# Kernel tuning notes

Hardware: AMD Instinct MI355X
Metric: run time of the kernel (lower is better)

## Reference

```python
import math
import jax, jax.numpy as jnp
import numpy as np

D = 2048
NH = 16
HD = D // NH
B_IMG = 32
H_ORIG, W_ORIG = 28, 36
POOL = 2
HF, WF = H_ORIG // POOL, W_ORIG // POOL  # 14, 18
T = HF * WF                              # 252 tokens per image
S_TOTAL = B_IMG * T                      # 8064
EPS = 1e-6


def setup_inputs() -> dict:
    key = jax.random.key(0)
    ks = jax.random.split(key, 12)
    w = lambda k, shp: jax.random.normal(k, shp, dtype=jnp.float32) * 0.02
    return {
        'semantic_hidden': jax.random.normal(ks[0], (1, S_TOTAL, D), jnp.float32),
        'vggt_features': jax.random.normal(ks[1], (1, S_TOTAL, D), jnp.float32),
        'grid_thw': jnp.tile(jnp.array([[1, H_ORIG, W_ORIG]], dtype=jnp.int64), (B_IMG, 1)),
        'ln1_w': jnp.ones((D,), jnp.float32), 'ln1_b': jnp.zeros((D,), jnp.float32),
        'ln2_w': jnp.ones((D,), jnp.float32), 'ln2_b': jnp.zeros((D,), jnp.float32),
        'Wq': w(ks[2], (D, D)), 'Wk': w(ks[3], (D, D)),
        'Wv': w(ks[4], (D, D)), 'Wo': w(ks[5], (D, D)),
        'imp_w1': w(ks[6], (D // 4, D)), 'imp_b1': jnp.zeros((D // 4,), jnp.float32),
        'imp_w2': w(ks[7], (1, D // 4)), 'imp_b2': jnp.zeros((1,), jnp.float32),
        'gate_w': w(ks[8], (NH // 2, D)), 'gate_b': jnp.zeros((NH // 2,), jnp.float32),
        'gate': jnp.asarray(0.5, jnp.float32),  # torch init is 0.0 (output would be all-zero); use 0.5 for a meaningful baseline
    }


def _layernorm(x, w, b):
    mu = jnp.mean(x, axis=-1, keepdims=True)
    var = jnp.var(x, axis=-1, keepdims=True)
    return (x - mu) * jax.lax.rsqrt(var + EPS) * w + b


def _spatial_bias(h_feat, w_feat, dtype):
    y = jnp.arange(h_feat, dtype=dtype)
    x = jnp.arange(w_feat, dtype=dtype)
    gy, gx = jnp.meshgrid(y, x, indexing='ij')
    coords = jnp.stack([gy.reshape(-1), gx.reshape(-1)], axis=-1)  # [N, 2]
    diff = coords[:, None, :] - coords[None, :, :]
    dist = jnp.sqrt(jnp.sum(diff * diff, axis=-1))  # [N, N]
    diag_len = math.sqrt(h_feat ** 2 + w_feat ** 2) + 1e-6
    return -dist / diag_len


def reference(semantic_hidden, vggt_features, grid_thw, ln1_w, ln1_b, ln2_w, ln2_b,
              Wq, Wk, Wv, Wo, imp_w1, imp_b1, imp_w2, imp_b2, gate_w, gate_b, gate):
    sem = _layernorm(semantic_hidden, ln1_w, ln1_b)
    vgg = _layernorm(vggt_features, ln2_w, ln2_b)
    B_orig, S_total, Dm = sem.shape

    # grid_thw is a static host constant -> Python ints (shapes must be static)
    h_feat = int(np.asarray(grid_thw)[0, 1]) // POOL
    w_feat = int(np.asarray(grid_thw)[0, 2]) // POOL
    tokens = h_feat * w_feat
    num_images = S_total // tokens

    q_in = sem.reshape(num_images, tokens, Dm)   # [B, S, D]
    kv_in = vgg.reshape(num_images, tokens, Dm)
    B, S = num_images, tokens

    q = (q_in @ Wq.T).reshape(B, S, NH, HD).transpose(0, 2, 1, 3)   # [B, H, S, hd]
    k = (kv_in @ Wk.T).reshape(B, S, NH, HD).transpose(0, 2, 1, 3)
    v = (kv_in @ Wv.T).reshape(B, S, NH, HD).transpose(0, 2, 1, 3)

    attn = jnp.einsum('bhqd,bhkd->bhqk', q, k) / math.sqrt(HD)       # [B, H, S, S]

    # spatial bias on first half of heads, gated per (image, query)
    sp_bias = _spatial_bias(h_feat, w_feat, q.dtype)                 # [S, S]
    gate_score = jax.nn.sigmoid(q_in @ gate_w.T + gate_b)            # [B, S, H/2]
    gate_score = gate_score.transpose(0, 2, 1)[..., None]            # [B, H/2, S, 1]
    split = NH // 2
    attn = attn.at[:, :split].add(sp_bias[None, None] * gate_score)

    # importance gate: log-importance bias over keys, shared across heads
    hidden = jax.nn.relu(q_in @ imp_w1.T + imp_b1)
    importance = jax.nn.sigmoid(hidden @ imp_w2.T + imp_b2)          # [B, S, 1]
    attn = attn + jnp.log(importance + 0.1).reshape(B, 1, 1, S)

    probs = jax.nn.softmax(attn, axis=-1)
    out = jnp.einsum('bhqk,bhkd->bhqd', probs, v)                    # [B, H, S, hd]
    out = out.transpose(0, 2, 1, 3).reshape(B, S, Dm)
    out = out.reshape(B_orig, S_total, Dm) @ Wo.T
    return jnp.tanh(gate) * out
```

## Files before the change

kernel.cpp:

```cpp
#include <hip/hip_runtime.h>
#include <hip/hip_bf16.h>
#include <math.h>

typedef __bf16 bf16_t;
typedef __bf16 bf16x8 __attribute__((ext_vector_type(8)));
typedef float f32x4v __attribute__((ext_vector_type(4)));
typedef unsigned short ushort_t;

#define SL_TOTAL 8064
#define SL_PAD 8192
#define DMODEL 2048
#define NHEAD 16
#define HDIM 128
#define SEQ 252

__device__ __forceinline__ bf16_t f2bf(float f) {
  unsigned u = __builtin_bit_cast(unsigned, f);
  u += 0x7fffu + ((u >> 16) & 1u);
  ushort_t h = (ushort_t)(u >> 16);
  return __builtin_bit_cast(bf16_t, h);
}
__device__ __forceinline__ float bf2f(bf16_t b) {
  unsigned u = ((unsigned)__builtin_bit_cast(ushort_t, b)) << 16;
  return __builtin_bit_cast(float, u);
}

__global__ __launch_bounds__(256) void cvt4_kernel(const float* __restrict__ s0,
                                                   const float* __restrict__ s1,
                                                   const float* __restrict__ s2,
                                                   const float* __restrict__ s3,
                                                   bf16_t* __restrict__ d0,
                                                   bf16_t* __restrict__ d1,
                                                   bf16_t* __restrict__ d2,
                                                   bf16_t* __restrict__ d3) {
  const float* src; bf16_t* dst;
  switch (blockIdx.y) {
    case 0: src = s0; dst = d0; break;
    case 1: src = s1; dst = d1; break;
    case 2: src = s2; dst = d2; break;
    default: src = s3; dst = d3; break;
  }
  int i = (blockIdx.x * 256 + threadIdx.x) * 8;
  float4 a = *(const float4*)(src + i);
  float4 b = *(const float4*)(src + i + 4);
  bf16x8 o;
  o[0] = f2bf(a.x); o[1] = f2bf(a.y); o[2] = f2bf(a.z); o[3] = f2bf(a.w);
  o[4] = f2bf(b.x); o[5] = f2bf(b.y); o[6] = f2bf(b.z); o[7] = f2bf(b.w);
  *(bf16x8*)(dst + i) = o;
}

__global__ __launch_bounds__(256) void cvt_kernel(const float* __restrict__ src,
                                                  bf16_t* __restrict__ dst, int n) {
  int i = (blockIdx.x * 256 + threadIdx.x) * 8;
  if (i >= n) return;
  float4 a = *(const float4*)(src + i);
  float4 b = *(const float4*)(src + i + 4);
  bf16x8 o;
  o[0] = f2bf(a.x); o[1] = f2bf(a.y); o[2] = f2bf(a.z); o[3] = f2bf(a.w);
  o[4] = f2bf(b.x); o[5] = f2bf(b.y); o[6] = f2bf(b.z); o[7] = f2bf(b.w);
  *(bf16x8*)(dst + i) = o;
}

__global__ __launch_bounds__(256) void ln_kernel(
    const float* __restrict__ sem, const float* __restrict__ vgg,
    const float* __restrict__ w1, const float* __restrict__ b1,
    const float* __restrict__ w2, const float* __restrict__ b2,
    bf16_t* __restrict__ o1, bf16_t* __restrict__ o2) {
  const float* x; const float* w; const float* bb; bf16_t* o;
  int row = blockIdx.x;
  if (blockIdx.y == 0) { x = sem; w = w1; bb = b1; o = o1; }
  else                 { x = vgg; w = w2; bb = b2; o = o2; }
  x += (size_t)row * DMODEL; o += (size_t)row * DMODEL;
  int t = threadIdx.x, wid = t >> 6, lane = t & 63;
  float4 va = *(const float4*)(x + t * 8);
  float4 vb = *(const float4*)(x + t * 8 + 4);
  float s  = va.x + va.y + va.z + va.w + vb.x + vb.y + vb.z + vb.w;
  float ss = va.x*va.x + va.y*va.y + va.z*va.z + va.w*va.w
           + vb.x*vb.x + vb.y*vb.y + vb.z*vb.z + vb.w*vb.w;
  #pragma unroll
  for (int m = 1; m < 64; m <<= 1) { s += __shfl_xor(s, m); ss += __shfl_xor(ss, m); }
  __shared__ float rs[4], rss[4];
  if (lane == 0) { rs[wid] = s; rss[wid] = ss; }
  __syncthreads();
  float st = rs[0] + rs[1] + rs[2] + rs[3];
  float sst = rss[0] + rss[1] + rss[2] + rss[3];
  float mu = st * (1.0f / 2048.0f);
  float var = sst * (1.0f / 2048.0f) - mu * mu;
  float rstd = rsqrtf(var + 1e-6f);
  float4 wa = *(const float4*)(w + t * 8);
  float4 wb = *(const float4*)(w + t * 8 + 4);
  float4 ba = *(const float4*)(bb + t * 8);
  float4 bb4 = *(const float4*)(bb + t * 8 + 4);
  bf16x8 ov;
  ov[0] = f2bf((va.x - mu) * rstd * wa.x + ba.x);
  ov[1] = f2bf((va.y - mu) * rstd * wa.y + ba.y);
  ov[2] = f2bf((va.z - mu) * rstd * wa.z + ba.z);
  ov[3] = f2bf((va.w - mu) * rstd * wa.w + ba.w);
  ov[4] = f2bf((vb.x - mu) * rstd * wb.x + bb4.x);
  ov[5] = f2bf((vb.y - mu) * rstd * wb.y + bb4.y);
  ov[6] = f2bf((vb.z - mu) * rstd * wb.z + bb4.z);
  ov[7] = f2bf((vb.w - mu) * rstd * wb.w + bb4.w);
  *(bf16x8*)(o + t * 8) = ov;
}

template <int EPI>
__global__ __launch_bounds__(512, 2) void gemm256(
    const bf16_t* __restrict__ A, const bf16_t* __restrict__ B,
    void* __restrict__ C, void* __restrict__ C2,
    const float* __restrict__ gatep,
    int Mreal, int N, int K, int nnt) {
  __shared__ bf16_t As[2][256 * 64];
  __shared__ bf16_t Bs[2][256 * 64];
  const int nblk = gridDim.x;
  const int orig = blockIdx.x;
  const int qd = nblk >> 3, rr = nblk & 7, xc = orig & 7, lin = orig >> 3;
  const int wg = (xc < rr ? xc * (qd + 1) : rr * (qd + 1) + (xc - rr) * qd) + lin;
  const int mtile = wg / nnt, ntile = wg - mtile * nnt;
  const int m0 = mtile * 256, n0 = ntile * 256;

  const int tid = threadIdx.x;
  const int wid = tid >> 6, lane = tid & 63;
  const int l15 = lane & 15, l4 = lane >> 4;
  const int wr = wid >> 2, wc = wid & 3;
  const int srow = lane >> 3;
  const int scol = 8 * ((lane & 7) ^ srow);

  f32x4v acc[8][4] = {};
  const int NKT = K >> 6;

  auto gload = [&](const bf16_t* g, bf16_t* l) {
    __builtin_amdgcn_global_load_lds((const __attribute__((address_space(1))) unsigned int*)g,
        (__attribute__((address_space(3))) unsigned int*)l, 16, 0, 0);
  };
  auto stageA4 = [&](int kt) {
    bf16_t* an = As[kt & 1];
    const int k0 = kt << 6;
    #pragma unroll
    for (int q = 0; q < 4; ++q) {
      int chunk = wr * 16 + wc * 4 + q;
      int row = chunk * 8 + srow;
      gload(A + (size_t)(m0 + row) * K + k0 + scol, an + chunk * 512);
    }
  };
  auto stageB4 = [&](int kt) {
    bf16_t* bn = Bs[kt & 1];
    const int k0 = kt << 6;
    #pragma unroll
    for (int q = 0; q < 4; ++q) {
      int chunk = wc * 8 + wr * 4 + q;
      int row = chunk * 8 + srow;
      gload(B + (size_t)(n0 + row) * K + k0 + scol, bn + chunk * 512);
    }
  };
  auto ld_a = [&](const bf16_t* as, int ks, int mi) -> bf16x8 {
    int row = wr * 128 + mi * 16 + l15;
    int cb = ks * 64 + l4 * 16;
    return *(const bf16x8*)((const char*)as + row * 128 + (cb ^ ((row & 7) << 4)));
  };
  auto ld_b = [&](const bf16_t* bs, int ks, int ni) -> bf16x8 {
    int row = wc * 64 + ni * 16 + l15;
    int cb = ks * 64 + l4 * 16;
    return *(const bf16x8*)((const char*)bs + row * 128 + (cb ^ ((row & 7) << 4)));
  };

  stageA4(0); stageB4(0); stageA4(1);
  asm volatile("s_waitcnt vmcnt(4)" ::: "memory");
  __builtin_amdgcn_s_barrier();

  for (int t = 0; t < NKT; ++t) {
    const bf16_t* as = As[t & 1];
    const bf16_t* bs = Bs[t & 1];
    bf16x8 afr[8], bfr[2];

    #pragma unroll
    for (int mi = 0; mi < 8; ++mi) afr[mi] = ld_a(as, 0, mi);
    bfr[0] = ld_b(bs, 0, 0); bfr[1] = ld_b(bs, 0, 1);
    if (t + 1 < NKT) stageB4(t + 1);
    __builtin_amdgcn_s_barrier();
    asm volatile("s_waitcnt lgkmcnt(0)" ::: "memory");
    __builtin_amdgcn_s_setprio(1);
    #pragma unroll
    for (int mi = 0; mi < 8; ++mi) {
      acc[mi][0] = __builtin_amdgcn_mfma_f32_16x16x32_bf16(afr[mi], bfr[0], acc[mi][0], 0, 0, 0);
      acc[mi][1] = __builtin_amdgcn_mfma_f32_16x16x32_bf16(afr[mi], bfr[1], acc[mi][1], 0, 0, 0);
    }
    __builtin_amdgcn_s_setprio(0);
    __builtin_amdgcn_s_barrier();

    bfr[0] = ld_b(bs, 0, 2); bfr[1] = ld_b(bs, 0, 3);
    __builtin_amdgcn_s_barrier();
    asm volatile("s_waitcnt lgkmcnt(0)" ::: "memory");
    __builtin_amdgcn_s_setprio(1);
    #pragma unroll
    for (int mi = 0; mi < 8; ++mi) {
      acc[mi][2] = __builtin_amdgcn_mfma_f32_16x16x32_bf16(afr[mi], bfr[0], acc[mi][2], 0, 0, 0);
      acc[mi][3] = __builtin_amdgcn_mfma_f32_16x16x32_bf16(afr[mi], bfr[1], acc[mi][3], 0, 0, 0);
    }
    __builtin_amdgcn_s_setprio(0);
    __builtin_amdgcn_s_barrier();

    #pragma unroll
    for (int mi = 0; mi < 8; ++mi) afr[mi] = ld_a(as, 1, mi);
    bfr[0] = ld_b(bs, 1, 0); bfr[1] = ld_b(bs, 1, 1);
    __builtin_amdgcn_s_barrier();
    asm volatile("s_waitcnt lgkmcnt(0)" ::: "memory");
    __builtin_amdgcn_s_setprio(1);
    #pragma unroll
    for (int mi = 0; mi < 8; ++mi) {
      acc[mi][0] = __builtin_amdgcn_mfma_f32_16x16x32_bf16(afr[mi], bfr[0], acc[mi][0], 0, 0, 0);
      acc[mi][1] = __builtin_amdgcn_mfma_f32_16x16x32_bf16(afr[mi], bfr[1], acc[mi][1], 0, 0, 0);
    }
    __builtin_amdgcn_s_setprio(0);
    __builtin_amdgcn_s_barrier();

    bfr[0] = ld_b(bs, 1, 2); bfr[1] = ld_b(bs, 1, 3);
    if (t + 2 < NKT) stageA4(t + 2);
    __builtin_amdgcn_s_barrier();
    asm volatile("s_waitcnt lgkmcnt(0)" ::: "memory");
    __builtin_amdgcn_s_setprio(1);
    #pragma unroll
    for (int mi = 0; mi < 8; ++mi) {
      acc[mi][2] = __builtin_amdgcn_mfma_f32_16x16x32_bf16(afr[mi], bfr[0], acc[mi][2], 0, 0, 0);
      acc[mi][3] = __builtin_amdgcn_mfma_f32_16x16x32_bf16(afr[mi], bfr[1], acc[mi][3], 0, 0, 0);
    }
    __builtin_amdgcn_s_setprio(0);
    if (t + 2 < NKT)      asm volatile("s_waitcnt vmcnt(4)" ::: "memory");
    else if (t + 1 < NKT) asm volatile("s_waitcnt vmcnt(0)" ::: "memory");
    __builtin_amdgcn_s_barrier();
  }

  float scale = 1.0f;
  if (EPI == 2) scale = tanhf(gatep[0]);
  bf16_t* Cb = (bf16_t*)C;
  int colbase = n0;
  int ldc = N;
  if (EPI == 3) {
    ldc = 2048;
    if (n0 >= 2048) { Cb = (bf16_t*)C2; colbase = n0 - 2048; }
  }
  #pragma unroll
  for (int mi = 0; mi < 8; ++mi) {
    #pragma unroll
    for (int ni = 0; ni < 4; ++ni) {
      int c = colbase + wc * 64 + ni * 16 + l15;
      #pragma unroll
      for (int j = 0; j < 4; ++j) {
        int r = m0 + wr * 128 + mi * 16 + 4 * l4 + j;
        if (r >= Mreal) continue;
        float v = acc[mi][ni][j];
        if (EPI == 2) ((float*)C)[(size_t)r * N + c] = v * scale;
        else Cb[(size_t)r * ldc + c] = f2bf(v);
      }
    }
  }
}

template <int EPI>
__global__ __launch_bounds__(256, 2) void gemm_bt(
    const bf16_t* __restrict__ A, const bf16_t* __restrict__ B,
    void* __restrict__ C, void* __restrict__ C2,
    const float* __restrict__ bias, const float* __restrict__ gatep,
    int M, int N, int K, int nnt) {
  __shared__ bf16_t As[2][128 * 64];
  __shared__ bf16_t Bs[2][128 * 64];
  const int nblk = gridDim.x;
  const int orig = blockIdx.x;
  const int qd = nblk >> 3, rr = nblk & 7, xc = orig & 7, lin = orig >> 3;
  const int wg = (xc < rr ? xc * (qd + 1) : rr * (qd + 1) + (xc - rr) * qd) + lin;
  const int mtile = wg / nnt;
  const int ntile = wg - mtile * nnt;
  const int m0 = mtile * 128, n0 = ntile * 128;

  const int tid = threadIdx.x;
  const int wid = tid >> 6, lane = tid & 63;
  const int l15 = lane & 15, l4 = lane >> 4;
  const int wm = (wid >> 1) * 64, wn = (wid & 1) * 64;
  const int srow = lane >> 3;
  const int scol = 8 * ((lane & 7) ^ (lane >> 3));

  f32x4v acc[4][4] = {};
  const int nkt = K >> 6;

  auto stage = [&](int kt, int buf) {
    const int k0 = kt << 6;
    #pragma unroll
    for (int it = 0; it < 4; ++it) {
      int chunk = wid + 4 * it;
      int row = chunk * 8 + srow;
      const bf16_t* ga = A + (size_t)(m0 + row) * K + k0 + scol;
      const bf16_t* gb = B + (size_t)(n0 + row) * K + k0 + scol;
      bf16_t* la = &As[buf][chunk * 512];
      bf16_t* lb = &Bs[buf][chunk * 512];
      __builtin_amdgcn_global_load_lds((const __attribute__((address_space(1))) unsigned int*)ga,
                                       (__attribute__((address_space(3))) unsigned int*)la, 16, 0, 0);
      __builtin_amdgcn_global_load_lds((const __attribute__((address_space(1))) unsigned int*)gb,
                                       (__attribute__((address_space(3))) unsigned int*)lb, 16, 0, 0);
    }
  };

  stage(0, 0);
  for (int kt = 0; kt < nkt; ++kt) {
    int buf = kt & 1;
    __syncthreads();
    if (kt + 1 < nkt) stage(kt + 1, buf ^ 1);
    const char* as = (const char*)As[buf];
    const char* bs = (const char*)Bs[buf];
    #pragma unroll
    for (int ki = 0; ki < 2; ++ki) {
      int cb = ki * 64 + l4 * 16;
      bf16x8 af[4], bfv[4];
      #pragma unroll
      for (int mi = 0; mi < 4; ++mi) {
        int row = wm + mi * 16 + l15;
        af[mi] = *(const bf16x8*)(as + row * 128 + (cb ^ ((row & 7) << 4)));
      }
      #pragma unroll
      for (int ni = 0; ni < 4; ++ni) {
        int row = wn + ni * 16 + l15;
        bfv[ni] = *(const bf16x8*)(bs + row * 128 + (cb ^ ((row & 7) << 4)));
      }
      #pragma unroll
      for (int mi = 0; mi < 4; ++mi)
        #pragma unroll
        for (int ni = 0; ni < 4; ++ni)
          acc[mi][ni] = __builtin_amdgcn_mfma_f32_16x16x32_bf16(af[mi], bfv[ni], acc[mi][ni], 0, 0, 0);
    }
    __syncthreads();
  }

  #pragma unroll
  for (int mi = 0; mi < 4; ++mi) {
    #pragma unroll
    for (int ni = 0; ni < 4; ++ni) {
      int c = n0 + wn + ni * 16 + l15;
      #pragma unroll
      for (int j = 0; j < 4; ++j) {
        int r = m0 + wm + mi * 16 + 4 * l4 + j;
        float v = acc[mi][ni][j];
        if (EPI == 1) { v += bias[c]; v = v > 0.0f ? v : 0.0f; }
        ((bf16_t*)C)[(size_t)r * N + c] = f2bf(v);
      }
    }
  }
}

__global__ __launch_bounds__(256) void gate_kernel(const bf16_t* __restrict__ a,
                                                   const float* __restrict__ gw,
                                                   const float* __restrict__ gb,
                                                   float* __restrict__ gs) {
  int r0 = blockIdx.x * 4;
  int t = threadIdx.x;
  int j = t >> 5, lt = t & 31;
  const float* wr = gw + (size_t)j * DMODEL;
  float sum[4] = {0.0f, 0.0f, 0.0f, 0.0f};
  #pragma unroll
  for (int u = 0; u < 8; ++u) {
    int i = lt * 8 + u * 256;
    float4 w0 = *(const float4*)(wr + i);
    float4 w1 = *(const float4*)(wr + i + 4);
    #pragma unroll
    for (int r = 0; r < 4; ++r) {
      bf16x8 av = *(const bf16x8*)(a + (size_t)(r0 + r) * DMODEL + i);
      sum[r] += bf2f(av[0]) * w0.x + bf2f(av[1]) * w0.y + bf2f(av[2]) * w0.z + bf2f(av[3]) * w0.w
              + bf2f(av[4]) * w1.x + bf2f(av[5]) * w1.y + bf2f(av[6]) * w1.z + bf2f(av[7]) * w1.w;
    }
  }
  #pragma unroll
  for (int m = 1; m < 32; m <<= 1) {
    #pragma unroll
    for (int r = 0; r < 4; ++r) sum[r] += __shfl_xor(sum[r], m);
  }
  if (lt == 0) {
    #pragma unroll
    for (int r = 0; r < 4; ++r)
      gs[(size_t)(r0 + r) * 8 + j] = 1.0f / (1.0f + __expf(-(sum[r] + gb[j])));
  }
}

__global__ __launch_bounds__(256) void imp_kernel(const bf16_t* __restrict__ hid,
                                                  const float* __restrict__ w2,
                                                  const float* __restrict__ b2,
                                                  float* __restrict__ kb) {
  int row = blockIdx.x * 4 + (threadIdx.x >> 6);
  int lane = threadIdx.x & 63;
  const bf16_t* hr = hid + (size_t)row * 512;
  bf16x8 hv = *(const bf16x8*)(hr + lane * 8);
  float sum = 0.0f;
  #pragma unroll
  for (int i = 0; i < 8; ++i) sum += bf2f(hv[i]) * w2[lane * 8 + i];
  #pragma unroll
  for (int m = 1; m < 64; m <<= 1) sum += __shfl_xor(sum, m);
  if (lane == 0) {
    float imp = 1.0f / (1.0f + __expf(-(sum + b2[0])));
    kb[row] = logf(imp + 0.1f);
  }
}

__global__ __launch_bounds__(512, 1) void attn_kernel(
    const bf16_t* __restrict__ Q, const bf16_t* __restrict__ K,
    const bf16_t* __restrict__ V, const float* __restrict__ gs,
    const float* __restrict__ kb, bf16_t* __restrict__ O) {
  __shared__ bf16_t Kt[64 * 128];
  __shared__ bf16_t Vt[128 * 64];
  __shared__ bf16_t Pl[8][32 * 72];
  __shared__ float kyf[256], kxf[256], kbl[256];

  const int bi = blockIdx.x >> 4;
  const int h = blockIdx.x & 15;
  const int tid = threadIdx.x;
  const int wid = tid >> 6;
  const int lane = tid & 63;
  const int l15 = lane & 15, l4 = lane >> 4;
  const bool hs = (h < 8);

  for (int i = tid; i < 256; i += 512) {
    kyf[i] = (float)(i / 18);
    kxf[i] = (float)(i % 18);
    int kk = i < SEQ ? i : SEQ - 1;
    kbl[i] = kb[bi * SEQ + kk];
  }

  const int q0 = wid * 32;
  bf16x8 qf[2][4];
  #pragma unroll
  for (int mi = 0; mi < 2; ++mi) {
    int q = q0 + mi * 16 + l15; if (q >= SEQ) q = SEQ - 1;
    const bf16_t* qp = Q + (size_t)(bi * SEQ + q) * DMODEL + h * HDIM;
    #pragma unroll
    for (int ki = 0; ki < 4; ++ki) qf[mi][ki] = *(const bf16x8*)(qp + ki * 32 + l4 * 8);
  }

  const float invdiag = 1.0f / (sqrtf(520.0f) + 1e-6f);
  float gsd[2][4], qyv[2][4], qxv[2][4];
  #pragma unroll
  for (int mi = 0; mi < 2; ++mi)
    #pragma unroll
    for (int j = 0; j < 4; ++j) {
      int q = q0 + mi * 16 + 4 * l4 + j;
      int qc = q < SEQ ? q : SEQ - 1;
      gsd[mi][j] = hs ? gs[(size_t)(bi * SEQ + qc) * 8 + h] * invdiag : 0.0f;
      qyv[mi][j] = (float)(q / 18);
      qxv[mi][j] = (float)(q % 18);
    }

  f32x4v oacc[2][8] = {};
  f32x4v osum[2] = {};
  const float scl = 0.08838834764831845f;
  bf16_t* Plw = &Pl[wid][0];
  bf16x8 vones;
  #pragma unroll
  for (int i = 0; i < 8; ++i) vones[i] = f2bf(1.0f);

  for (int t = 0; t < 4; ++t) {
    __syncthreads();
    #pragma unroll
    for (int rep = 0; rep < 2; ++rep) {
      int s = tid + rep * 512;
      int row = s >> 4, cb = s & 15;
      int kk = t * 64 + row;
      uint4 val = make_uint4(0, 0, 0, 0);
      if (kk < SEQ) val = *(const uint4*)(K + (size_t)(bi * SEQ + kk) * DMODEL + h * HDIM + cb * 8);
      *(uint4*)((char*)Kt + row * 256 + ((cb * 16) ^ ((row & 7) << 4))) = val;
    }
    {
      int kp = tid >> 4, db = tid & 15;
      int k0i = t * 64 + kp * 2, k1i = k0i + 1;
      uint4 a = make_uint4(0, 0, 0, 0), c4 = make_uint4(0, 0, 0, 0);
      if (k0i < SEQ) a = *(const uint4*)(V + (size_t)(bi * SEQ + k0i) * DMODEL + h * HDIM + db * 8);
      if (k1i < SEQ) c4 = *(const uint4*)(V + (size_t)(bi * SEQ + k1i) * DMODEL + h * HDIM + db * 8);
      const ushort_t* au = (const ushort_t*)&a;
      const ushort_t* cu = (const ushort_t*)&c4;
      #pragma unroll
      for (int i = 0; i < 8; ++i) {
        int d = db * 8 + i;
        unsigned pv = (unsigned)au[i] | ((unsigned)cu[i] << 16);
        *(unsigned*)((char*)Vt + d * 128 + ((kp * 4) ^ ((d & 7) << 4))) = pv;
      }
    }
    __syncthreads();

    f32x4v sc[2][4] = {};
    #pragma unroll
    for (int ki = 0; ki < 4; ++ki) {
      bf16x8 kf[4];
      #pragma unroll
      for (int ni = 0; ni < 4; ++ni) {
        int row = ni * 16 + l15;
        kf[ni] = *(const bf16x8*)((char*)Kt + row * 256 + ((ki * 64 + l4 * 16) ^ ((row & 7) << 4)));
      }
      #pragma unroll
      for (int mi = 0; mi < 2; ++mi)
        #pragma unroll
        for (int ni = 0; ni < 4; ++ni)
          sc[mi][ni] = __builtin_amdgcn_mfma_f32_16x16x32_bf16(qf[mi][ki], kf[ni], sc[mi][ni], 0, 0, 0);
    }

    #pragma unroll
    for (int mi = 0; mi < 2; ++mi) {
      #pragma unroll
      for (int j = 0; j < 4; ++j) {
        int prow = mi * 16 + 4 * l4 + j;
        #pragma unroll
        for (int ni = 0; ni < 4; ++ni) {
          int kk = t * 64 + ni * 16 + l15;
          float s = sc[mi][ni][j] * scl + kbl[kk];
          if (hs) {
            float dy = qyv[mi][j] - kyf[kk];
            float dx = qxv[mi][j] - kxf[kk];
            s -= sqrtf(dy * dy + dx * dx) * gsd[mi][j];
          }
          float p = (kk < SEQ) ? __expf(s) : 0.0f;
          Plw[prow * 72 + ni * 16 + l15] = f2bf(p);
        }
      }
    }

    #pragma unroll
    for (int ks = 0; ks < 2; ++ks) {
      bf16x8 pf[2];
      #pragma unroll
      for (int mi = 0; mi < 2; ++mi)
        pf[mi] = *(const bf16x8*)(Plw + (mi * 16 + l15) * 72 + ks * 32 + l4 * 8);
      #pragma unroll
      for (int mi = 0; mi < 2; ++mi)
        osum[mi] = __builtin_amdgcn_mfma_f32_16x16x32_bf16(pf[mi], vones, osum[mi], 0, 0, 0);
      #pragma unroll
      for (int di = 0; di < 8; ++di) {
        int d = di * 16 + l15;
        bf16x8 vf = *(const bf16x8*)((char*)Vt + d * 128 + ((ks * 64 + l4 * 16) ^ ((d & 7) << 4)));
        #pragma unroll
        for (int mi = 0; mi < 2; ++mi)
          oacc[mi][di] = __builtin_amdgcn_mfma_f32_16x16x32_bf16(pf[mi], vf, oacc[mi][di], 0, 0, 0);
      }
    }
  }

  #pragma unroll
  for (int mi = 0; mi < 2; ++mi) {
    #pragma unroll
    for (int j = 0; j < 4; ++j) {
      int q = q0 + mi * 16 + 4 * l4 + j;
      if (q >= SEQ) continue;
      float inv = 1.0f / osum[mi][j];
      bf16_t* op = O + (size_t)(bi * SEQ + q) * DMODEL + h * HDIM;
      #pragma unroll
      for (int di = 0; di < 8; ++di)
        op[di * 16 + l15] = f2bf(oacc[mi][di][j] * inv);
    }
  }
}

extern "C" void kernel_launch(void* const* d_in, const int* in_sizes, int n_in,
                              void* d_out, int out_size, void* d_ws, size_t ws_size,
                              hipStream_t stream) {
  const float* sem  = (const float*)d_in[0];
  const float* vgg  = (const float*)d_in[1];
  const float* ln1w = (const float*)d_in[3];
  const float* ln1b = (const float*)d_in[4];
  const float* ln2w = (const float*)d_in[5];
  const float* ln2b = (const float*)d_in[6];
  const float* Wq   = (const float*)d_in[7];
  const float* Wk   = (const float*)d_in[8];
  const float* Wv   = (const float*)d_in[9];
  const float* Wo   = (const float*)d_in[10];
  const float* w1   = (const float*)d_in[11];
  const float* b1   = (const float*)d_in[12];
  const float* w2   = (const float*)d_in[13];
  const float* b2   = (const float*)d_in[14];
  const float* gw   = (const float*)d_in[15];
  const float* gb   = (const float*)d_in[16];
  const float* gate = (const float*)d_in[17];

  char* ws = (char*)d_ws;
  const size_t SZ_W    = 8388608;
  const size_t SZ_PAD  = 33554432;
  const size_t SZ_ACT  = 33030144;
  bf16_t* Wqb  = (bf16_t*)(ws + 0);
  bf16_t* Wkb  = (bf16_t*)(ws + SZ_W);
  bf16_t* Wvb  = (bf16_t*)(ws + 2 * SZ_W);
  bf16_t* Wob  = (bf16_t*)(ws + 3 * SZ_W);
  bf16_t* w1b  = (bf16_t*)(ws + 4 * SZ_W);
  bf16_t* semb = (bf16_t*)(ws + 4 * SZ_W + 2097152);
  bf16_t* vggb = (bf16_t*)(ws + 4 * SZ_W + 2097152 + SZ_PAD);
  bf16_t* Vb   = (bf16_t*)(ws + 4 * SZ_W + 2097152 + 2 * SZ_PAD);
  bf16_t* hidb = (bf16_t*)(ws + 4 * SZ_W + 2097152 + 2 * SZ_PAD + SZ_ACT);
  float*  gsb  = (float*)(ws + 4 * SZ_W + 2097152 + 2 * SZ_PAD + SZ_ACT + 8257536);
  float*  kbb  = (float*)(ws + 4 * SZ_W + 2097152 + 2 * SZ_PAD + SZ_ACT + 8257536 + 258048);
  bf16_t* Qb = (bf16_t*)d_out;
  bf16_t* Kb = (bf16_t*)((char*)d_out + SZ_ACT);
  bf16_t* attnb = semb;

  cvt4_kernel<<<dim3(2048, 4), 256, 0, stream>>>(Wq, Wk, Wv, Wo, Wqb, Wkb, Wvb, Wob);
  cvt_kernel<<<512, 256, 0, stream>>>(w1, w1b, 1048576);
  ln_kernel<<<dim3(8064, 2), 256, 0, stream>>>(sem, vgg, ln1w, ln1b, ln2w, ln2b, semb, vggb);

  gemm256<0><<<256, 512, 0, stream>>>(semb, Wqb, Qb, nullptr, nullptr,
                                      8064, 2048, 2048, 8);
  gemm256<3><<<512, 512, 0, stream>>>(vggb, Wkb, Kb, Vb, nullptr,
                                      8064, 4096, 2048, 16);
  gemm_bt<1><<<252, 256, 0, stream>>>(semb, w1b, hidb, nullptr, b1, nullptr,
                                      8064, 512, 2048, 4);

  gate_kernel<<<2016, 256, 0, stream>>>(semb, gw, gb, gsb);
  imp_kernel<<<2016, 256, 0, stream>>>(hidb, w2, b2, kbb);

  attn_kernel<<<512, 512, 0, stream>>>(Qb, Kb, Vb, gsb, kbb, attnb);

  gemm256<2><<<256, 512, 0, stream>>>(attnb, Wob, d_out, nullptr, gate,
                                      8064, 2048, 2048, 8);
}
```

Measured before the change: 467.2 us.

## Double-buffer V tiles in LDS and read K fragments directly from global

The attention kernel now prefetches the next V tile into registers while the current tile is processed, and writes it into a double-buffered LDS array, so one barrier per iteration replaces two. K is no longer staged in shared memory; each wave loads its MFMA K fragments straight from global memory, relying on L1/L2 reuse across the 8 waves. This removes load latency and a sync from the critical path, at the cost of redundant global K reads per wave and more register pressure from the fully unrolled loop.

```diff
diff --git a/kernel.cpp b/kernel.cpp
--- a/kernel.cpp
+++ b/kernel.cpp
@@ -400,8 +400,7 @@
     const bf16_t* __restrict__ Q, const bf16_t* __restrict__ K,
     const bf16_t* __restrict__ V, const float* __restrict__ gs,
     const float* __restrict__ kb, bf16_t* __restrict__ O) {
-  __shared__ bf16_t Kt[64 * 128];
-  __shared__ bf16_t Vt[128 * 64];
+  __shared__ bf16_t Vt[2][128 * 64];
   __shared__ bf16_t Pl[8][32 * 72];
   __shared__ float kyf[256], kxf[256], kbl[256];
 
@@ -420,6 +419,9 @@
     kbl[i] = kb[bi * SEQ + kk];
   }
 
+  const bf16_t* Kbase = K + (size_t)bi * SEQ * DMODEL + h * HDIM;
+  const bf16_t* Vbase = V + (size_t)bi * SEQ * DMODEL + h * HDIM;
+
   const int q0 = wid * 32;
   bf16x8 qf[2][4];
   #pragma unroll
@@ -443,6 +445,27 @@
       qxv[mi][j] = (float)(q % 18);
     }
 
+  const int kp = tid >> 4, db = tid & 15;
+  uint4 va0, vb0, va1, vb1;
+  auto loadV = [&](int t, uint4& a, uint4& b) {
+    int k0i = t * 64 + kp * 2, k1i = k0i + 1;
+    a = make_uint4(0, 0, 0, 0); b = make_uint4(0, 0, 0, 0);
+    if (k0i < SEQ) a = *(const uint4*)(Vbase + (size_t)k0i * DMODEL + db * 8);
+    if (k1i < SEQ) b = *(const uint4*)(Vbase + (size_t)k1i * DMODEL + db * 8);
+  };
+  auto writeV = [&](int buf, uint4 a, uint4 b) {
+    const ushort_t* au = (const ushort_t*)&a;
+    const ushort_t* cu = (const ushort_t*)&b;
+    #pragma unroll
+    for (int i = 0; i < 8; ++i) {
+      int d = db * 8 + i;
+      unsigned pv = (unsigned)au[i] | ((unsigned)cu[i] << 16);
+      *(unsigned*)((char*)Vt[buf] + d * 128 + ((kp * 4) ^ ((d & 7) << 4))) = pv;
+    }
+  };
+
+  loadV(0, va0, vb0);
+
   f32x4v oacc[2][8] = {};
   f32x4v osum[2] = {};
   const float scl = 0.08838834764831845f;
@@ -451,32 +474,10 @@
   #pragma unroll
   for (int i = 0; i < 8; ++i) vones[i] = f2bf(1.0f);
 
+  #pragma unroll
   for (int t = 0; t < 4; ++t) {
-    __syncthreads();
-    #pragma unroll
-    for (int rep = 0; rep < 2; ++rep) {
-      int s = tid + rep * 512;
-      int row = s >> 4, cb = s & 15;
-      int kk = t * 64 + row;
-      uint4 val = make_uint4(0, 0, 0, 0);
-      if (kk < SEQ) val = *(const uint4*)(K + (size_t)(bi * SEQ + kk) * DMODEL + h * HDIM + cb * 8);
-      *(uint4*)((char*)Kt + row * 256 + ((cb * 16) ^ ((row & 7) << 4))) = val;
-    }
-    {
-      int kp = tid >> 4, db = tid & 15;
-      int k0i = t * 64 + kp * 2, k1i = k0i + 1;
-      uint4 a = make_uint4(0, 0, 0, 0), c4 = make_uint4(0, 0, 0, 0);
-      if (k0i < SEQ) a = *(const uint4*)(V + (size_t)(bi * SEQ + k0i) * DMODEL + h * HDIM + db * 8);
-      if (k1i < SEQ) c4 = *(const uint4*)(V + (size_t)(bi * SEQ + k1i) * DMODEL + h * HDIM + db * 8);
-      const ushort_t* au = (const ushort_t*)&a;
-      const ushort_t* cu = (const ushort_t*)&c4;
-      #pragma unroll
-      for (int i = 0; i < 8; ++i) {
-        int d = db * 8 + i;
-        unsigned pv = (unsigned)au[i] | ((unsigned)cu[i] << 16);
-        *(unsigned*)((char*)Vt + d * 128 + ((kp * 4) ^ ((d & 7) << 4))) = pv;
-      }
-    }
+    writeV(t & 1, va0, vb0);
+    if (t + 1 < 4) loadV(t + 1, va1, vb1);
     __syncthreads();
 
     f32x4v sc[2][4] = {};
@@ -485,8 +486,9 @@
       bf16x8 kf[4];
       #pragma unroll
       for (int ni = 0; ni < 4; ++ni) {
-        int row = ni * 16 + l15;
-        kf[ni] = *(const bf16x8*)((char*)Kt + row * 256 + ((ki * 64 + l4 * 16) ^ ((row & 7) << 4)));
+        int kk = t * 64 + ni * 16 + l15;
+        int kc = kk < SEQ ? kk : SEQ - 1;
+        kf[ni] = *(const bf16x8*)(Kbase + (size_t)kc * DMODEL + ki * 32 + l4 * 8);
       }
       #pragma unroll
       for (int mi = 0; mi < 2; ++mi)
@@ -527,12 +529,13 @@
       #pragma unroll
       for (int di = 0; di < 8; ++di) {
         int d = di * 16 + l15;
-        bf16x8 vf = *(const bf16x8*)((char*)Vt + d * 128 + ((ks * 64 + l4 * 16) ^ ((d & 7) << 4)));
+        bf16x8 vf = *(const bf16x8*)((char*)Vt[t & 1] + d * 128 + ((ks * 64 + l4 * 16) ^ ((d & 7) << 4)));
         #pragma unroll
         for (int mi = 0; mi < 2; ++mi)
           oacc[mi][di] = __builtin_amdgcn_mfma_f32_16x16x32_bf16(pf[mi], vf, oacc[mi][di], 0, 0, 0);
       }
     }
+    va0 = va1; vb0 = vb1;
   }
 
   #pragma unroll
```

Result: slower. 495.0 us (+6.0%).
